# Performance work log

Measured on AMD Instinct MI355X. Metric: run time of the kernel, lower is better.

The kernel has to match this reference:

```python
import jax, jax.numpy as jnp
import numpy as np

N_NODES = 50000
N_EDGES = 400000
H = 64          # node hidden state dim (entities_dimensions['node'])
E_DIM = 8       # edge_params dim (message.extra_parameters)
MSG_HID = 128   # message-creation MLP hidden width
RD_HID = 128    # readout hidden width
T = 2           # message-passing steps


def setup_inputs() -> dict:
    key = jax.random.key(0)
    ks = jax.random.split(key, 12)
    def w(k, shape):
        return jax.random.normal(k, shape, dtype=jnp.float32) * 0.05
    return {
        "node_feats": jax.random.normal(ks[0], (N_NODES, H), dtype=jnp.float32),
        "edge_feats": jax.random.normal(ks[1], (N_EDGES, E_DIM), dtype=jnp.float32),
        "edge_src": jax.random.randint(ks[2], (N_EDGES,), 0, N_NODES),
        "edge_dst": jax.random.randint(ks[3], (N_EDGES,), 0, N_NODES),
        # message creation MLP: concat(hs_src, hs_dst, edge_params) -> relu -> H
        "W_msg1": w(ks[4], (2 * H + E_DIM, MSG_HID)),
        "b_msg1": jnp.zeros((MSG_HID,), jnp.float32),
        "W_msg2": w(ks[5], (MSG_HID, H)),
        "b_msg2": jnp.zeros((H,), jnp.float32),
        # GRU cell update (keras GRUCell convention, reset_after=False)
        "W_x": w(ks[6], (H, 3 * H)),
        "W_h": w(ks[7], (H, 3 * H)),
        "b_gru": jnp.zeros((3 * H,), jnp.float32),
        # readout MLP: H -> relu -> 1
        "W_r1": w(ks[8], (H, RD_HID)),
        "b_r1": jnp.zeros((RD_HID,), jnp.float32),
        "W_r2": w(ks[9], (RD_HID, 1)),
        "b_r2": jnp.zeros((1,), jnp.float32),
    }


def _gru_cell(h, x, W_x, W_h, b):
    # gates order: update (z), reset (r), candidate (h~) — keras convention
    gx = x @ W_x + b
    gh = h @ W_h
    xz, xr, xh = jnp.split(gx, 3, axis=-1)
    hz, hr, hh = jnp.split(gh, 3, axis=-1)
    z = jax.nn.sigmoid(xz + hz)
    r = jax.nn.sigmoid(xr + hr)
    hc = jnp.tanh(xh + r * hh)
    return z * h + (1.0 - z) * hc


def reference(node_feats, edge_feats, edge_src, edge_dst,
              W_msg1, b_msg1, W_msg2, b_msg2,
              W_x, W_h, b_gru, W_r1, b_r1, W_r2, b_r2):
    h = node_feats  # [N, H] hidden states initialized from entity features
    for _ in range(T):
        # gather source/destination node states per edge: [E, H]
        src_h = h[edge_src]
        dst_h = h[edge_dst]
        m_in = jnp.concatenate([src_h, dst_h, edge_feats], axis=-1)  # [E, 2H+E_DIM]
        m = jax.nn.relu(m_in @ W_msg1 + b_msg1) @ W_msg2 + b_msg2    # [E, H]
        # scatter-sum aggregation to destination nodes: [N, H]
        agg = jax.ops.segment_sum(m, edge_dst, num_segments=N_NODES)
        # recurrent (GRU) node-state update
        h = _gru_cell(h, agg, W_x, W_h, b_gru)
    # readout MLP on final hidden states
    out = jax.nn.relu(h @ W_r1 + b_r1) @ W_r2 + b_r2  # [N, 1]
    return out
```

## Files before the change

kernel.cpp:

```cpp
#include <hip/hip_runtime.h>
#include <hip/hip_bf16.h>

#define NN 50000
#define NE 400000
#define NPAIR 12500
#define NCH 196
#define NPAD 50176

typedef __bf16 bf16_t;
typedef __bf16 bf16x4 __attribute__((ext_vector_type(4)));
typedef __bf16 bf16x8 __attribute__((ext_vector_type(8)));
typedef float  floatx4 __attribute__((ext_vector_type(4)));

static __device__ __forceinline__ floatx4 mfma16(bf16x8 a, bf16x8 b, floatx4 c) {
    return __builtin_amdgcn_mfma_f32_16x16x32_bf16(a, b, c, 0, 0, 0);
}
static __device__ __forceinline__ float sigm_f(float x) {
    return 1.f / (1.f + __expf(-x));
}
static __device__ __forceinline__ float tanh_f(float x) {
    return 1.f - 2.f / (__expf(2.f * x) + 1.f);
}
static __device__ __forceinline__ bf16x8 cvt8(const float* sp) {
    float4 f0 = *(const float4*)sp;
    float4 f1 = *(const float4*)(sp + 4);
    bf16x8 v;
    v[0] = (bf16_t)f0.x; v[1] = (bf16_t)f0.y; v[2] = (bf16_t)f0.z; v[3] = (bf16_t)f0.w;
    v[4] = (bf16_t)f1.x; v[5] = (bf16_t)f1.y; v[6] = (bf16_t)f1.z; v[7] = (bf16_t)f1.w;
    return v;
}

__global__ __launch_bounds__(256) void prep_kernel(
    const float* __restrict__ nf,
    const float* __restrict__ Wm1, const float* __restrict__ Wm2,
    const float* __restrict__ Wx,  const float* __restrict__ Wh,
    const float* __restrict__ Wr1,
    bf16_t* __restrict__ hb,
    bf16_t* __restrict__ W1f, bf16_t* __restrict__ W2f,
    bf16_t* __restrict__ Wxt, bf16_t* __restrict__ Wht,
    bf16_t* __restrict__ Wr1f)
{
    int u = blockIdx.x * 256 + threadIdx.x;
    if (u < 800000) {
        float4 v = *(const float4*)(nf + (size_t)u * 4);
        bf16x4 o;
        o[0] = (bf16_t)v.x; o[1] = (bf16_t)v.y; o[2] = (bf16_t)v.z; o[3] = (bf16_t)v.w;
        *(bf16x4*)(hb + (size_t)u * 4) = o;
        return;
    }
    u -= 800000;
    if (u < 20480) {
        int j = u & 7, l = (u >> 3) & 63, rem = u >> 9;
        int ks = rem % 5, nt = rem / 5;
        int n = nt * 16 + (l & 15);
        int k = ks * 32 + (l >> 4) * 8 + j;
        W1f[u] = (k < 136) ? (bf16_t)Wm1[k * 128 + n] : (bf16_t)0.f;
        return;
    }
    u -= 20480;
    if (u < 8192) {
        int j = u & 7, l = (u >> 3) & 63, rem = u >> 9;
        int kg = rem & 3, nt = rem >> 2;
        int n = nt * 16 + (l & 15);
        int k = kg * 32 + (l >> 4) * 8 + j;
        W2f[u] = (bf16_t)Wm2[k * 64 + n];
        return;
    }
    u -= 8192;
    if (u < 12288) {
        int n = u >> 6, k = u & 63;
        Wxt[u] = (bf16_t)Wx[k * 192 + n];
        return;
    }
    u -= 12288;
    if (u < 12288) {
        int n = u >> 6, k = u & 63;
        Wht[u] = (bf16_t)Wh[k * 192 + n];
        return;
    }
    u -= 12288;
    if (u < 8192) {
        int j = u & 7, l = (u >> 3) & 63, rem = u >> 9;
        int kg = rem & 1, nt = rem >> 1;
        int n = nt * 16 + (l & 15);
        int k = kg * 32 + (l >> 4) * 8 + j;
        Wr1f[u] = (bf16_t)Wr1[k * 128 + n];
    }
}

__global__ __launch_bounds__(256) void hist_kernel(
    const int* __restrict__ edst, int* __restrict__ deg)
{
    int e = blockIdx.x * 256 + threadIdx.x;
    if (e < NE) atomicAdd(&deg[edst[e]], 1);
}

__global__ __launch_bounds__(256) void scanA_kernel(
    const int* __restrict__ deg, int* __restrict__ chunkSums)
{
    __shared__ int s[256];
    int i = blockIdx.x * 256 + threadIdx.x;
    s[threadIdx.x] = deg[i];
    __syncthreads();
    for (int st = 128; st >= 1; st >>= 1) {
        if (threadIdx.x < st) s[threadIdx.x] += s[threadIdx.x + st];
        __syncthreads();
    }
    if (threadIdx.x == 0) chunkSums[blockIdx.x] = s[0];
}

__global__ __launch_bounds__(256) void scanB_kernel(
    const int* __restrict__ chunkSums, int* __restrict__ chunkOff)
{
    __shared__ int s[256];
    int t = threadIdx.x;
    int v = (t < NCH) ? chunkSums[t] : 0;
    s[t] = v;
    __syncthreads();
    for (int st = 1; st < 256; st <<= 1) {
        int add = (t >= st) ? s[t - st] : 0;
        __syncthreads();
        s[t] += add;
        __syncthreads();
    }
    if (t < NCH) chunkOff[t] = s[t] - v;
}

__global__ __launch_bounds__(256) void scanC_kernel(
    const int* __restrict__ deg, const int* __restrict__ chunkOff,
    int* __restrict__ cursor)
{
    __shared__ int s[256];
    int t = threadIdx.x;
    int i = blockIdx.x * 256 + t;
    int v = deg[i];
    s[t] = v;
    __syncthreads();
    for (int st = 1; st < 256; st <<= 1) {
        int add = (t >= st) ? s[t - st] : 0;
        __syncthreads();
        s[t] += add;
        __syncthreads();
    }
    cursor[i] = chunkOff[blockIdx.x] + s[t] - v;
}

__global__ __launch_bounds__(256) void scatter_kernel(
    const int* __restrict__ esrc, const int* __restrict__ edst,
    const float* __restrict__ ef,
    int* __restrict__ cursor, int* __restrict__ srcs, int* __restrict__ dsts,
    bf16_t* __restrict__ efpb)
{
    int e = blockIdx.x * 256 + threadIdx.x;
    if (e >= NE) return;
    int d = edst[e];
    int p = atomicAdd(&cursor[d], 1);
    srcs[p] = esrc[e];
    dsts[p] = d;
    float4 a = *(const float4*)(ef + (size_t)e * 8);
    float4 b = *(const float4*)(ef + (size_t)e * 8 + 4);
    bf16x8 v;
    v[0] = (bf16_t)a.x; v[1] = (bf16_t)a.y; v[2] = (bf16_t)a.z; v[3] = (bf16_t)a.w;
    v[4] = (bf16_t)b.x; v[5] = (bf16_t)b.y; v[6] = (bf16_t)b.z; v[7] = (bf16_t)b.w;
    *(bf16x8*)(efpb + (size_t)p * 8) = v;
}

__global__ __launch_bounds__(256) void edge_kernel(
    const bf16_t* __restrict__ hb, const bf16_t* __restrict__ efpb,
    const int* __restrict__ srcs, const int* __restrict__ dsts,
    const bf16_t* __restrict__ W1f, const bf16_t* __restrict__ W2f,
    const float* __restrict__ b1f, const float* __restrict__ b2f,
    bf16_t* __restrict__ mb)
{
    __shared__ __attribute__((aligned(16))) bf16_t w1s[20480];
    __shared__ __attribute__((aligned(16))) bf16_t w2s[8192];
    __shared__ __attribute__((aligned(16))) bf16_t hq[4][32 * 36];

    const int tid = threadIdx.x;
    {
        const uint4* s1 = (const uint4*)W1f;
        uint4* d1 = (uint4*)w1s;
        #pragma unroll
        for (int i = 0; i < 10; i++) d1[tid + i * 256] = s1[tid + i * 256];
        const uint4* s2 = (const uint4*)W2f;
        uint4* d2 = (uint4*)w2s;
        #pragma unroll
        for (int i = 0; i < 4; i++) d2[tid + i * 256] = s2[tid + i * 256];
    }
    __syncthreads();

    const int lane = tid & 63;
    const int wv   = tid >> 6;
    const int l15  = lane & 15;
    const int quad = lane >> 4;

    float b1r[8], b2r[4];
    #pragma unroll
    for (int nt = 0; nt < 8; nt++) b1r[nt] = b1f[nt * 16 + l15];
    #pragma unroll
    for (int nt = 0; nt < 4; nt++) b2r[nt] = b2f[nt * 16 + l15];

    const int WTOT = gridDim.x * 4;
    int p = blockIdx.x * 4 + wv;

    bf16x8 af0[5], af1[5];
    {
        int base = p * 32;
        int r0 = base + l15, r1 = base + 16 + l15;
        int si0 = srcs[r0], di0 = dsts[r0];
        int si1 = srcs[r1], di1 = dsts[r1];
        const bf16_t* sp0 = hb + (size_t)si0 * 64 + quad * 8;
        const bf16_t* dp0 = hb + (size_t)di0 * 64 + quad * 8;
        const bf16_t* sp1 = hb + (size_t)si1 * 64 + quad * 8;
        const bf16_t* dp1 = hb + (size_t)di1 * 64 + quad * 8;
        af0[0] = *(const bf16x8*)sp0;  af0[1] = *(const bf16x8*)(sp0 + 32);
        af0[2] = *(const bf16x8*)dp0;  af0[3] = *(const bf16x8*)(dp0 + 32);
        af1[0] = *(const bf16x8*)sp1;  af1[1] = *(const bf16x8*)(sp1 + 32);
        af1[2] = *(const bf16x8*)dp1;  af1[3] = *(const bf16x8*)(dp1 + 32);
        if (quad == 0) {
            af0[4] = *(const bf16x8*)(efpb + (size_t)r0 * 8);
            af1[4] = *(const bf16x8*)(efpb + (size_t)r1 * 8);
        } else {
            #pragma unroll
            for (int q = 0; q < 8; q++) { af0[4][q] = (bf16_t)0.f; af1[4][q] = (bf16_t)0.f; }
        }
    }

    while (true) {
        int pn = p + WTOT;
        int pp = (pn < NPAIR) ? pn : p;
        int nbase = pp * 32;
        int nr0 = nbase + l15, nr1 = nbase + 16 + l15;
        int si0n = srcs[nr0], di0n = dsts[nr0];
        int si1n = srcs[nr1], di1n = dsts[nr1];

        floatx4 oa0[4], oa1[4];
        #pragma unroll
        for (int nt = 0; nt < 4; nt++) {
            oa0[nt].x=0.f; oa0[nt].y=0.f; oa0[nt].z=0.f; oa0[nt].w=0.f;
            oa1[nt].x=0.f; oa1[nt].y=0.f; oa1[nt].z=0.f; oa1[nt].w=0.f;
        }

        #pragma unroll
        for (int q = 0; q < 4; q++) {
            floatx4 ac0[2], ac1[2];
            #pragma unroll
            for (int nt = 0; nt < 2; nt++) {
                ac0[nt].x=0.f; ac0[nt].y=0.f; ac0[nt].z=0.f; ac0[nt].w=0.f;
                ac1[nt].x=0.f; ac1[nt].y=0.f; ac1[nt].z=0.f; ac1[nt].w=0.f;
            }
            #pragma unroll
            for (int nt = 0; nt < 2; nt++) {
                int gnt = q * 2 + nt;
                #pragma unroll
                for (int ks = 0; ks < 5; ks++) {
                    bf16x8 b = *(const bf16x8*)(w1s + ((gnt * 5 + ks) * 64 + lane) * 8);
                    ac0[nt] = mfma16(af0[ks], b, ac0[nt]);
                    ac1[nt] = mfma16(af1[ks], b, ac1[nt]);
                }
            }
            #pragma unroll
            for (int nt = 0; nt < 2; nt++) {
                float bb = b1r[q * 2 + nt];
                #pragma unroll
                for (int r = 0; r < 4; r++) {
                    float v0 = fmaxf(ac0[nt][r] + bb, 0.f);
                    float v1 = fmaxf(ac1[nt][r] + bb, 0.f);
                    hq[wv][(quad * 4 + r) * 36 + nt * 16 + l15]      = (bf16_t)v0;
                    hq[wv][(16 + quad * 4 + r) * 36 + nt * 16 + l15] = (bf16_t)v1;
                }
            }
            bf16x8 hf0 = *(const bf16x8*)(hq[wv] + l15 * 36 + quad * 8);
            bf16x8 hf1 = *(const bf16x8*)(hq[wv] + (16 + l15) * 36 + quad * 8);
            #pragma unroll
            for (int nt = 0; nt < 4; nt++) {
                bf16x8 w2 = *(const bf16x8*)(w2s + ((nt * 4 + q) * 64 + lane) * 8);
                oa0[nt] = mfma16(hf0, w2, oa0[nt]);
                oa1[nt] = mfma16(hf1, w2, oa1[nt]);
            }
        }

        int base = p * 32;
        {
            const bf16_t* sp0 = hb + (size_t)si0n * 64 + quad * 8;
            const bf16_t* dp0 = hb + (size_t)di0n * 64 + quad * 8;
            const bf16_t* sp1 = hb + (size_t)si1n * 64 + quad * 8;
            const bf16_t* dp1 = hb + (size_t)di1n * 64 + quad * 8;
            af0[0] = *(const bf16x8*)sp0;  af0[1] = *(const bf16x8*)(sp0 + 32);
            af0[2] = *(const bf16x8*)dp0;  af0[3] = *(const bf16x8*)(dp0 + 32);
            af1[0] = *(const bf16x8*)sp1;  af1[1] = *(const bf16x8*)(sp1 + 32);
            af1[2] = *(const bf16x8*)dp1;  af1[3] = *(const bf16x8*)(dp1 + 32);
            if (quad == 0) {
                af0[4] = *(const bf16x8*)(efpb + (size_t)nr0 * 8);
                af1[4] = *(const bf16x8*)(efpb + (size_t)nr1 * 8);
            }
        }

        #pragma unroll
        for (int nt = 0; nt < 4; nt++) {
            int col = nt * 16 + l15;
            float bb = b2r[nt];
            #pragma unroll
            for (int r = 0; r < 4; r++) {
                int row0 = base + quad * 4 + r;
                int row1 = base + 16 + quad * 4 + r;
                mb[(size_t)row0 * 64 + col] = (bf16_t)(oa0[nt][r] + bb);
                mb[(size_t)row1 * 64 + col] = (bf16_t)(oa1[nt][r] + bb);
            }
        }

        if (pn >= NPAIR) break;
        p = pn;
    }
}

__global__ __launch_bounds__(256) void agg_kernel(
    const bf16_t* __restrict__ mb, const int* __restrict__ deg,
    const int* __restrict__ cursor, bf16_t* __restrict__ aggb)
{
    const int node = blockIdx.x * 4 + (threadIdx.x >> 6);
    if (node >= NN) return;
    const int lane = threadIdx.x & 63;
    int dg  = deg[node];
    int end = cursor[node];
    int st  = end - dg;
    float s0 = 0.f, s1 = 0.f;
    int e = st;
    for (; e + 1 < end; e += 2) {
        s0 += (float)mb[(size_t)e * 64 + lane];
        s1 += (float)mb[(size_t)(e + 1) * 64 + lane];
    }
    if (e < end) s0 += (float)mb[(size_t)e * 64 + lane];
    aggb[(size_t)node * 64 + lane] = (bf16_t)(s0 + s1);
}

template<int LAST>
__global__ __launch_bounds__(256) void gru_kernel(
    const bf16_t* __restrict__ aggb, const float* __restrict__ h_in,
    float* __restrict__ h_out, bf16_t* __restrict__ hb_out,
    const bf16_t* __restrict__ Wxt, const bf16_t* __restrict__ Wht,
    const float* __restrict__ bg,
    const bf16_t* __restrict__ Wr1f, const float* __restrict__ br1,
    const float* __restrict__ Wr2, const float* __restrict__ br2,
    float* __restrict__ out)
{
    __shared__ __attribute__((aligned(16))) float  shd[64 * 68];
    __shared__ __attribute__((aligned(16))) bf16_t hb2[4][16 * 72];
    const int tid = threadIdx.x;
    const int n0  = blockIdx.x * 64;

    for (int idx = tid; idx < 64 * 16; idx += 256) {
        int i = idx >> 4, c = (idx & 15) * 4;
        int n = n0 + i; if (n >= NN) n = NN - 1;
        *(float4*)&shd[i * 68 + c] = *(const float4*)(h_in + (size_t)n * 64 + c);
    }
    __syncthreads();

    const int lane = tid & 63;
    const int wv   = tid >> 6;
    const int l15  = lane & 15;
    const int quad = lane >> 4;
    const int rowA = wv * 16 + l15;
    int nA = n0 + rowA; if (nA >= NN) nA = NN - 1;

    bf16x8 ax[2], ah[2];
    ax[0] = *(const bf16x8*)(aggb + (size_t)nA * 64 + quad * 8);
    ax[1] = *(const bf16x8*)(aggb + (size_t)nA * 64 + quad * 8 + 32);
    {
        const float* hp = shd + rowA * 68 + quad * 8;
        ah[0] = cvt8(hp);
        ah[1] = cvt8(hp + 32);
    }

    floatx4 az[4], ar[4], axh[4], ahh[4];
    #pragma unroll
    for (int nt = 0; nt < 4; nt++) {
        az[nt].x=0.f; az[nt].y=0.f; az[nt].z=0.f; az[nt].w=0.f;
        ar[nt].x=0.f; ar[nt].y=0.f; ar[nt].z=0.f; ar[nt].w=0.f;
        axh[nt].x=0.f; axh[nt].y=0.f; axh[nt].z=0.f; axh[nt].w=0.f;
        ahh[nt].x=0.f; ahh[nt].y=0.f; ahh[nt].z=0.f; ahh[nt].w=0.f;
    }
    #pragma unroll
    for (int nt = 0; nt < 4; nt++) {
        const bf16_t* bx_z = Wxt + (nt * 16 + l15) * 64 + quad * 8;
        const bf16_t* bh_z = Wht + (nt * 16 + l15) * 64 + quad * 8;
        const bf16_t* bx_r = bx_z + 64 * 64;
        const bf16_t* bh_r = bh_z + 64 * 64;
        const bf16_t* bx_h = bx_z + 128 * 64;
        const bf16_t* bh_h = bh_z + 128 * 64;
        az[nt]  = mfma16(ax[0], *(const bf16x8*)bx_z,        az[nt]);
        az[nt]  = mfma16(ax[1], *(const bf16x8*)(bx_z + 32), az[nt]);
        az[nt]  = mfma16(ah[0], *(const bf16x8*)bh_z,        az[nt]);
        az[nt]  = mfma16(ah[1], *(const bf16x8*)(bh_z + 32), az[nt]);
        ar[nt]  = mfma16(ax[0], *(const bf16x8*)bx_r,        ar[nt]);
        ar[nt]  = mfma16(ax[1], *(const bf16x8*)(bx_r + 32), ar[nt]);
        ar[nt]  = mfma16(ah[0], *(const bf16x8*)bh_r,        ar[nt]);
        ar[nt]  = mfma16(ah[1], *(const bf16x8*)(bh_r + 32), ar[nt]);
        axh[nt] = mfma16(ax[0], *(const bf16x8*)bx_h,        axh[nt]);
        axh[nt] = mfma16(ax[1], *(const bf16x8*)(bx_h + 32), axh[nt]);
        ahh[nt] = mfma16(ah[0], *(const bf16x8*)bh_h,        ahh[nt]);
        ahh[nt] = mfma16(ah[1], *(const bf16x8*)(bh_h + 32), ahh[nt]);
    }

    #pragma unroll
    for (int nt = 0; nt < 4; nt++) {
        int j = nt * 16 + l15;
        float bz = bg[j], brr = bg[64 + j], bh = bg[128 + j];
        #pragma unroll
        for (int r = 0; r < 4; r++) {
            int lrow = wv * 16 + quad * 4 + r;
            int n = n0 + lrow;
            float z  = sigm_f(az[nt][r] + bz);
            float rr = sigm_f(ar[nt][r] + brr);
            float hc = tanh_f(axh[nt][r] + bh + rr * ahh[nt][r]);
            float hold = shd[lrow * 68 + j];
            float hnew = z * hold + (1.f - z) * hc;
            if (LAST) {
                hb2[wv][(quad * 4 + r) * 72 + j] = (bf16_t)hnew;
            } else if (n < NN) {
                h_out[(size_t)n * 64 + j]  = hnew;
                hb_out[(size_t)n * 64 + j] = (bf16_t)hnew;
            }
        }
    }

    if (LAST) {
        bf16x8 a0 = *(const bf16x8*)(hb2[wv] + l15 * 72 + quad * 8);
        bf16x8 a1 = *(const bf16x8*)(hb2[wv] + l15 * 72 + quad * 8 + 32);
        floatx4 accR[8];
        #pragma unroll
        for (int nt = 0; nt < 8; nt++) { accR[nt].x=0.f; accR[nt].y=0.f; accR[nt].z=0.f; accR[nt].w=0.f; }
        #pragma unroll
        for (int nt = 0; nt < 8; nt++) {
            bf16x8 b0 = *(const bf16x8*)(Wr1f + ((nt * 2 + 0) * 64 + lane) * 8);
            bf16x8 b1 = *(const bf16x8*)(Wr1f + ((nt * 2 + 1) * 64 + lane) * 8);
            accR[nt] = mfma16(a0, b0, accR[nt]);
            accR[nt] = mfma16(a1, b1, accR[nt]);
        }
        float br1r[8], wr2r[8];
        #pragma unroll
        for (int nt = 0; nt < 8; nt++) {
            br1r[nt] = br1[nt * 16 + l15];
            wr2r[nt] = Wr2[nt * 16 + l15];
        }
        float br2v = br2[0];
        #pragma unroll
        for (int r = 0; r < 4; r++) {
            float p = 0.f;
            #pragma unroll
            for (int nt = 0; nt < 8; nt++)
                p += fmaxf(accR[nt][r] + br1r[nt], 0.f) * wr2r[nt];
            p += __shfl_xor(p, 1, 64);
            p += __shfl_xor(p, 2, 64);
            p += __shfl_xor(p, 4, 64);
            p += __shfl_xor(p, 8, 64);
            if (l15 == 0) {
                int n = n0 + wv * 16 + quad * 4 + r;
                if (n < NN) out[n] = p + br2v;
            }
        }
    }
}

extern "C" void kernel_launch(void* const* d_in, const int* in_sizes, int n_in,
                              void* d_out, int out_size, void* d_ws, size_t ws_size,
                              hipStream_t stream)
{
    const float* nf  = (const float*)d_in[0];
    const float* ef  = (const float*)d_in[1];
    const int* esrc  = (const int*)d_in[2];
    const int* edst  = (const int*)d_in[3];
    const float* Wm1 = (const float*)d_in[4];
    const float* bm1 = (const float*)d_in[5];
    const float* Wm2 = (const float*)d_in[6];
    const float* bm2 = (const float*)d_in[7];
    const float* Wx  = (const float*)d_in[8];
    const float* Wh  = (const float*)d_in[9];
    const float* bg  = (const float*)d_in[10];
    const float* Wr1 = (const float*)d_in[11];
    const float* br1 = (const float*)d_in[12];
    const float* Wr2 = (const float*)d_in[13];
    const float* br2 = (const float*)d_in[14];

    char* ws = (char*)d_ws;
    float*  hbuf   = (float*)(ws);
    bf16_t* hb     = (bf16_t*)(ws + 12800000);
    bf16_t* W1f    = (bf16_t*)(ws + 19200000);
    bf16_t* W2f    = (bf16_t*)(ws + 19240960);
    bf16_t* Wxt    = (bf16_t*)(ws + 19257344);
    bf16_t* Wht    = (bf16_t*)(ws + 19281920);
    bf16_t* Wr1f   = (bf16_t*)(ws + 19306496);
    int*    srcs   = (int*)(ws + 19322880);
    int*    dsts   = (int*)(ws + 20922880);
    bf16_t* efpb   = (bf16_t*)(ws + 22522880);
    int*    deg    = (int*)(ws + 28922880);
    int*    cursor = (int*)(ws + 29123584);
    int*    chunkS = (int*)(ws + 29324288);
    int*    chunkO = (int*)(ws + 29325312);
    bf16_t* aggb   = (bf16_t*)(ws + 29326336);
    bf16_t* mb     = (bf16_t*)(ws + 35726336);

    prep_kernel<<<3365, 256, 0, stream>>>(nf, Wm1, Wm2, Wx, Wh, Wr1,
                                          hb, W1f, W2f, Wxt, Wht, Wr1f);

    hipMemsetAsync(deg, 0, (size_t)NPAD * 4, stream);
    hist_kernel<<<(NE + 255) / 256, 256, 0, stream>>>(edst, deg);
    scanA_kernel<<<NCH, 256, 0, stream>>>(deg, chunkS);
    scanB_kernel<<<1, 256, 0, stream>>>(chunkS, chunkO);
    scanC_kernel<<<NCH, 256, 0, stream>>>(deg, chunkO, cursor);
    scatter_kernel<<<(NE + 255) / 256, 256, 0, stream>>>(esrc, edst, ef, cursor,
                                                         srcs, dsts, efpb);

    edge_kernel<<<1024, 256, 0, stream>>>(hb, efpb, srcs, dsts,
                                          W1f, W2f, bm1, bm2, mb);
    agg_kernel<<<(NN + 3) / 4, 256, 0, stream>>>(mb, deg, cursor, aggb);
    gru_kernel<0><<<(NN + 63) / 64, 256, 0, stream>>>(
        aggb, nf, hbuf, hb, Wxt, Wht, bg, Wr1f, br1, Wr2, br2, (float*)d_out);
    edge_kernel<<<1024, 256, 0, stream>>>(hb, efpb, srcs, dsts,
                                          W1f, W2f, bm1, bm2, mb);
    agg_kernel<<<(NN + 3) / 4, 256, 0, stream>>>(mb, deg, cursor, aggb);
    gru_kernel<1><<<(NN + 63) / 64, 256, 0, stream>>>(
        aggb, hbuf, nullptr, nullptr, Wxt, Wht, bg, Wr1f, br1, Wr2, br2,
        (float*)d_out);
}
```

Before: 324.6 us.

## Process 64 edges per wave, permute message columns, vectorize aggregation, fuse histogram

The edge kernel now processes four 16-row tiles (64 edges) per wave, so each shared-memory weight fragment feeds four MFMAs instead of two. The W2 columns are permuted so each lane writes a packed bf16x4 of messages and packed bf16x2 hidden values. The aggregation kernel reads bf16x4 per lane across four edges in parallel and reduces with shuffles. The degree histogram is folded into the prep kernel and the edge grid is halved. This raises register pressure per wave and leaves fewer waves for load balancing.

```diff
diff --git a/kernel.cpp b/kernel.cpp
--- a/kernel.cpp
+++ b/kernel.cpp
@@ -3,11 +3,12 @@
 
 #define NN 50000
 #define NE 400000
-#define NPAIR 12500
+#define NUNIT 6250
 #define NCH 196
 #define NPAD 50176
 
 typedef __bf16 bf16_t;
+typedef __bf16 bf16x2 __attribute__((ext_vector_type(2)));
 typedef __bf16 bf16x4 __attribute__((ext_vector_type(4)));
 typedef __bf16 bf16x8 __attribute__((ext_vector_type(8)));
 typedef float  floatx4 __attribute__((ext_vector_type(4)));
@@ -35,6 +36,7 @@
     const float* __restrict__ Wm1, const float* __restrict__ Wm2,
     const float* __restrict__ Wx,  const float* __restrict__ Wh,
     const float* __restrict__ Wr1,
+    const int* __restrict__ edst, int* __restrict__ deg,
     bf16_t* __restrict__ hb,
     bf16_t* __restrict__ W1f, bf16_t* __restrict__ W2f,
     bf16_t* __restrict__ Wxt, bf16_t* __restrict__ Wht,
@@ -62,7 +64,8 @@
         int j = u & 7, l = (u >> 3) & 63, rem = u >> 9;
         int kg = rem & 3, nt = rem >> 2;
         int n = nt * 16 + (l & 15);
-        int k = kg * 32 + (l >> 4) * 8 + j;
+        int local = (l >> 4) * 8 + j;
+        int k = kg * 32 + (local >> 1) + (local & 1) * 16;
         W2f[u] = (bf16_t)Wm2[k * 64 + n];
         return;
     }
@@ -85,14 +88,10 @@
         int n = nt * 16 + (l & 15);
         int k = kg * 32 + (l >> 4) * 8 + j;
         Wr1f[u] = (bf16_t)Wr1[k * 128 + n];
-    }
-}
-
-__global__ __launch_bounds__(256) void hist_kernel(
-    const int* __restrict__ edst, int* __restrict__ deg)
-{
-    int e = blockIdx.x * 256 + threadIdx.x;
-    if (e < NE) atomicAdd(&deg[edst[e]], 1);
+        return;
+    }
+    u -= 8192;
+    if (u < NE) atomicAdd(&deg[edst[u]], 1);
 }
 
 __global__ __launch_bounds__(256) void scanA_kernel(
@@ -165,7 +164,7 @@
     *(bf16x8*)(efpb + (size_t)p * 8) = v;
 }
 
-__global__ __launch_bounds__(256) void edge_kernel(
+__global__ __launch_bounds__(256, 2) void edge_kernel(
     const bf16_t* __restrict__ hb, const bf16_t* __restrict__ efpb,
     const int* __restrict__ srcs, const int* __restrict__ dsts,
     const bf16_t* __restrict__ W1f, const bf16_t* __restrict__ W2f,
@@ -174,7 +173,7 @@
 {
     __shared__ __attribute__((aligned(16))) bf16_t w1s[20480];
     __shared__ __attribute__((aligned(16))) bf16_t w2s[8192];
-    __shared__ __attribute__((aligned(16))) bf16_t hq[4][32 * 36];
+    __shared__ __attribute__((aligned(16))) bf16_t hq[4][64 * 36];
 
     const int tid = threadIdx.x;
     {
@@ -203,113 +202,117 @@
     const int WTOT = gridDim.x * 4;
     int p = blockIdx.x * 4 + wv;
 
-    bf16x8 af0[5], af1[5];
+    bf16x8 af[4][5];
     {
-        int base = p * 32;
-        int r0 = base + l15, r1 = base + 16 + l15;
-        int si0 = srcs[r0], di0 = dsts[r0];
-        int si1 = srcs[r1], di1 = dsts[r1];
-        const bf16_t* sp0 = hb + (size_t)si0 * 64 + quad * 8;
-        const bf16_t* dp0 = hb + (size_t)di0 * 64 + quad * 8;
-        const bf16_t* sp1 = hb + (size_t)si1 * 64 + quad * 8;
-        const bf16_t* dp1 = hb + (size_t)di1 * 64 + quad * 8;
-        af0[0] = *(const bf16x8*)sp0;  af0[1] = *(const bf16x8*)(sp0 + 32);
-        af0[2] = *(const bf16x8*)dp0;  af0[3] = *(const bf16x8*)(dp0 + 32);
-        af1[0] = *(const bf16x8*)sp1;  af1[1] = *(const bf16x8*)(sp1 + 32);
-        af1[2] = *(const bf16x8*)dp1;  af1[3] = *(const bf16x8*)(dp1 + 32);
-        if (quad == 0) {
-            af0[4] = *(const bf16x8*)(efpb + (size_t)r0 * 8);
-            af1[4] = *(const bf16x8*)(efpb + (size_t)r1 * 8);
-        } else {
-            #pragma unroll
-            for (int q = 0; q < 8; q++) { af0[4][q] = (bf16_t)0.f; af1[4][q] = (bf16_t)0.f; }
+        int base = p * 64;
+        #pragma unroll
+        for (int s = 0; s < 4; s++) {
+            int r = base + s * 16 + l15;
+            int si = srcs[r], di = dsts[r];
+            const bf16_t* sp = hb + (size_t)si * 64 + quad * 8;
+            const bf16_t* dp = hb + (size_t)di * 64 + quad * 8;
+            af[s][0] = *(const bf16x8*)sp;  af[s][1] = *(const bf16x8*)(sp + 32);
+            af[s][2] = *(const bf16x8*)dp;  af[s][3] = *(const bf16x8*)(dp + 32);
+            if (quad == 0) {
+                af[s][4] = *(const bf16x8*)(efpb + (size_t)r * 8);
+            } else {
+                #pragma unroll
+                for (int q = 0; q < 8; q++) af[s][4][q] = (bf16_t)0.f;
+            }
         }
     }
 
     while (true) {
         int pn = p + WTOT;
-        int pp = (pn < NPAIR) ? pn : p;
-        int nbase = pp * 32;
-        int nr0 = nbase + l15, nr1 = nbase + 16 + l15;
-        int si0n = srcs[nr0], di0n = dsts[nr0];
-        int si1n = srcs[nr1], di1n = dsts[nr1];
-
-        floatx4 oa0[4], oa1[4];
-        #pragma unroll
-        for (int nt = 0; nt < 4; nt++) {
-            oa0[nt].x=0.f; oa0[nt].y=0.f; oa0[nt].z=0.f; oa0[nt].w=0.f;
-            oa1[nt].x=0.f; oa1[nt].y=0.f; oa1[nt].z=0.f; oa1[nt].w=0.f;
-        }
+        int pp = (pn < NUNIT) ? pn : p;
+        int nbase = pp * 64;
+        int sin[4], din[4];
+        #pragma unroll
+        for (int s = 0; s < 4; s++) {
+            sin[s] = srcs[nbase + s * 16 + l15];
+            din[s] = dsts[nbase + s * 16 + l15];
+        }
+
+        floatx4 oa[4][4];
+        #pragma unroll
+        for (int s = 0; s < 4; s++)
+            #pragma unroll
+            for (int nt = 0; nt < 4; nt++) {
+                oa[s][nt].x=0.f; oa[s][nt].y=0.f; oa[s][nt].z=0.f; oa[s][nt].w=0.f;
+            }
 
         #pragma unroll
         for (int q = 0; q < 4; q++) {
-            floatx4 ac0[2], ac1[2];
-            #pragma unroll
-            for (int nt = 0; nt < 2; nt++) {
-                ac0[nt].x=0.f; ac0[nt].y=0.f; ac0[nt].z=0.f; ac0[nt].w=0.f;
-                ac1[nt].x=0.f; ac1[nt].y=0.f; ac1[nt].z=0.f; ac1[nt].w=0.f;
-            }
+            floatx4 ac[4][2];
+            #pragma unroll
+            for (int s = 0; s < 4; s++)
+                #pragma unroll
+                for (int nt = 0; nt < 2; nt++) {
+                    ac[s][nt].x=0.f; ac[s][nt].y=0.f; ac[s][nt].z=0.f; ac[s][nt].w=0.f;
+                }
             #pragma unroll
             for (int nt = 0; nt < 2; nt++) {
                 int gnt = q * 2 + nt;
                 #pragma unroll
                 for (int ks = 0; ks < 5; ks++) {
                     bf16x8 b = *(const bf16x8*)(w1s + ((gnt * 5 + ks) * 64 + lane) * 8);
-                    ac0[nt] = mfma16(af0[ks], b, ac0[nt]);
-                    ac1[nt] = mfma16(af1[ks], b, ac1[nt]);
+                    #pragma unroll
+                    for (int s = 0; s < 4; s++)
+                        ac[s][nt] = mfma16(af[s][ks], b, ac[s][nt]);
                 }
             }
-            #pragma unroll
-            for (int nt = 0; nt < 2; nt++) {
-                float bb = b1r[q * 2 + nt];
+            {
+                float bb0 = b1r[q * 2 + 0], bb1 = b1r[q * 2 + 1];
                 #pragma unroll
-                for (int r = 0; r < 4; r++) {
-                    float v0 = fmaxf(ac0[nt][r] + bb, 0.f);
-                    float v1 = fmaxf(ac1[nt][r] + bb, 0.f);
-                    hq[wv][(quad * 4 + r) * 36 + nt * 16 + l15]      = (bf16_t)v0;
-                    hq[wv][(16 + quad * 4 + r) * 36 + nt * 16 + l15] = (bf16_t)v1;
+                for (int s = 0; s < 4; s++) {
+                    #pragma unroll
+                    for (int r = 0; r < 4; r++) {
+                        float v0 = fmaxf(ac[s][0][r] + bb0, 0.f);
+                        float v1 = fmaxf(ac[s][1][r] + bb1, 0.f);
+                        bf16x2 t; t[0] = (bf16_t)v0; t[1] = (bf16_t)v1;
+                        *(bf16x2*)(hq[wv] + (s * 16 + quad * 4 + r) * 36 + l15 * 2) = t;
+                    }
                 }
             }
-            bf16x8 hf0 = *(const bf16x8*)(hq[wv] + l15 * 36 + quad * 8);
-            bf16x8 hf1 = *(const bf16x8*)(hq[wv] + (16 + l15) * 36 + quad * 8);
+            bf16x8 hf[4];
+            #pragma unroll
+            for (int s = 0; s < 4; s++)
+                hf[s] = *(const bf16x8*)(hq[wv] + (s * 16 + l15) * 36 + quad * 8);
             #pragma unroll
             for (int nt = 0; nt < 4; nt++) {
                 bf16x8 w2 = *(const bf16x8*)(w2s + ((nt * 4 + q) * 64 + lane) * 8);
-                oa0[nt] = mfma16(hf0, w2, oa0[nt]);
-                oa1[nt] = mfma16(hf1, w2, oa1[nt]);
-            }
-        }
-
-        int base = p * 32;
-        {
-            const bf16_t* sp0 = hb + (size_t)si0n * 64 + quad * 8;
-            const bf16_t* dp0 = hb + (size_t)di0n * 64 + quad * 8;
-            const bf16_t* sp1 = hb + (size_t)si1n * 64 + quad * 8;
-            const bf16_t* dp1 = hb + (size_t)di1n * 64 + quad * 8;
-            af0[0] = *(const bf16x8*)sp0;  af0[1] = *(const bf16x8*)(sp0 + 32);
-            af0[2] = *(const bf16x8*)dp0;  af0[3] = *(const bf16x8*)(dp0 + 32);
-            af1[0] = *(const bf16x8*)sp1;  af1[1] = *(const bf16x8*)(sp1 + 32);
-            af1[2] = *(const bf16x8*)dp1;  af1[3] = *(const bf16x8*)(dp1 + 32);
-            if (quad == 0) {
-                af0[4] = *(const bf16x8*)(efpb + (size_t)nr0 * 8);
-                af1[4] = *(const bf16x8*)(efpb + (size_t)nr1 * 8);
-            }
-        }
-
-        #pragma unroll
-        for (int nt = 0; nt < 4; nt++) {
-            int col = nt * 16 + l15;
-            float bb = b2r[nt];
+                #pragma unroll
+                for (int s = 0; s < 4; s++)
+                    oa[s][nt] = mfma16(hf[s], w2, oa[s][nt]);
+            }
+        }
+
+        int base = p * 64;
+        #pragma unroll
+        for (int s = 0; s < 4; s++) {
+            const bf16_t* sp = hb + (size_t)sin[s] * 64 + quad * 8;
+            const bf16_t* dp = hb + (size_t)din[s] * 64 + quad * 8;
+            af[s][0] = *(const bf16x8*)sp;  af[s][1] = *(const bf16x8*)(sp + 32);
+            af[s][2] = *(const bf16x8*)dp;  af[s][3] = *(const bf16x8*)(dp + 32);
+            if (quad == 0)
+                af[s][4] = *(const bf16x8*)(efpb + (size_t)(nbase + s * 16 + l15) * 8);
+        }
+
+        #pragma unroll
+        for (int s = 0; s < 4; s++) {
             #pragma unroll
             for (int r = 0; r < 4; r++) {
-                int row0 = base + quad * 4 + r;
-                int row1 = base + 16 + quad * 4 + r;
-                mb[(size_t)row0 * 64 + col] = (bf16_t)(oa0[nt][r] + bb);
-                mb[(size_t)row1 * 64 + col] = (bf16_t)(oa1[nt][r] + bb);
-            }
-        }
-
-        if (pn >= NPAIR) break;
+                int row = base + s * 16 + quad * 4 + r;
+                bf16x4 t;
+                t[0] = (bf16_t)(oa[s][0][r] + b2r[0]);
+                t[1] = (bf16_t)(oa[s][1][r] + b2r[1]);
+                t[2] = (bf16_t)(oa[s][2][r] + b2r[2]);
+                t[3] = (bf16_t)(oa[s][3][r] + b2r[3]);
+                *(bf16x4*)(mb + (size_t)row * 64 + l15 * 4) = t;
+            }
+        }
+
+        if (pn >= NUNIT) break;
         p = pn;
     }
 }
@@ -321,17 +324,26 @@
     const int node = blockIdx.x * 4 + (threadIdx.x >> 6);
     if (node >= NN) return;
     const int lane = threadIdx.x & 63;
+    const int l15  = lane & 15;
+    const int quad = lane >> 4;
     int dg  = deg[node];
     int end = cursor[node];
     int st  = end - dg;
-    float s0 = 0.f, s1 = 0.f;
-    int e = st;
-    for (; e + 1 < end; e += 2) {
-        s0 += (float)mb[(size_t)e * 64 + lane];
-        s1 += (float)mb[(size_t)(e + 1) * 64 + lane];
-    }
-    if (e < end) s0 += (float)mb[(size_t)e * 64 + lane];
-    aggb[(size_t)node * 64 + lane] = (bf16_t)(s0 + s1);
+    float a0 = 0.f, a1 = 0.f, a2 = 0.f, a3 = 0.f;
+    for (int e = st + quad; e < end; e += 4) {
+        bf16x4 v = *(const bf16x4*)(mb + (size_t)e * 64 + l15 * 4);
+        a0 += (float)v[0]; a1 += (float)v[1]; a2 += (float)v[2]; a3 += (float)v[3];
+    }
+    a0 += __shfl_xor(a0, 16, 64); a0 += __shfl_xor(a0, 32, 64);
+    a1 += __shfl_xor(a1, 16, 64); a1 += __shfl_xor(a1, 32, 64);
+    a2 += __shfl_xor(a2, 16, 64); a2 += __shfl_xor(a2, 32, 64);
+    a3 += __shfl_xor(a3, 16, 64); a3 += __shfl_xor(a3, 32, 64);
+    if (quad == 0) {
+        aggb[(size_t)node * 64 +      l15] = (bf16_t)a0;
+        aggb[(size_t)node * 64 + 16 + l15] = (bf16_t)a1;
+        aggb[(size_t)node * 64 + 32 + l15] = (bf16_t)a2;
+        aggb[(size_t)node * 64 + 48 + l15] = (bf16_t)a3;
+    }
 }
 
 template<int LAST>
@@ -500,24 +512,23 @@
     bf16_t* aggb   = (bf16_t*)(ws + 29326336);
     bf16_t* mb     = (bf16_t*)(ws + 35726336);
 
-    prep_kernel<<<3365, 256, 0, stream>>>(nf, Wm1, Wm2, Wx, Wh, Wr1,
+    hipMemsetAsync(deg, 0, (size_t)NPAD * 4, stream);
+    prep_kernel<<<4928, 256, 0, stream>>>(nf, Wm1, Wm2, Wx, Wh, Wr1, edst, deg,
                                           hb, W1f, W2f, Wxt, Wht, Wr1f);
 
-    hipMemsetAsync(deg, 0, (size_t)NPAD * 4, stream);
-    hist_kernel<<<(NE + 255) / 256, 256, 0, stream>>>(edst, deg);
     scanA_kernel<<<NCH, 256, 0, stream>>>(deg, chunkS);
     scanB_kernel<<<1, 256, 0, stream>>>(chunkS, chunkO);
     scanC_kernel<<<NCH, 256, 0, stream>>>(deg, chunkO, cursor);
     scatter_kernel<<<(NE + 255) / 256, 256, 0, stream>>>(esrc, edst, ef, cursor,
                                                          srcs, dsts, efpb);
 
-    edge_kernel<<<1024, 256, 0, stream>>>(hb, efpb, srcs, dsts,
-                                          W1f, W2f, bm1, bm2, mb);
+    edge_kernel<<<512, 256, 0, stream>>>(hb, efpb, srcs, dsts,
+                                         W1f, W2f, bm1, bm2, mb);
     agg_kernel<<<(NN + 3) / 4, 256, 0, stream>>>(mb, deg, cursor, aggb);
     gru_kernel<0><<<(NN + 63) / 64, 256, 0, stream>>>(
         aggb, nf, hbuf, hb, Wxt, Wht, bg, Wr1f, br1, Wr2, br2, (float*)d_out);
-    edge_kernel<<<1024, 256, 0, stream>>>(hb, efpb, srcs, dsts,
-                                          W1f, W2f, bm1, bm2, mb);
+    edge_kernel<<<512, 256, 0, stream>>>(hb, efpb, srcs, dsts,
+                                         W1f, W2f, bm1, bm2, mb);
     agg_kernel<<<(NN + 3) / 4, 256, 0, stream>>>(mb, deg, cursor, aggb);
     gru_kernel<1><<<(NN + 63) / 64, 256, 0, stream>>>(
         aggb, hbuf, nullptr, nullptr, Wxt, Wht, bg, Wr1f, br1, Wr2, br2,
```

New measurement: 372.0 us. 14.6% more time.

## Drop W2 from LDS, pack hidden stores, fuse histogram into prep kernel

Applied to the files above, without the earlier changes.

The edge kernel no longer stages W_msg2 in shared memory; it reads the fragments straight from global memory, which should be L2-resident. This shrinks LDS use so that three blocks fit per CU (launch bounds 3, grid 768). The W2 fragment layout is permuted so each lane can write its two relu outputs to the hq tile as one bf16x2 store instead of two scalar stores. The degree histogram is folded into the prep kernel to remove a launch. The risk is higher latency from the global W2 loads inside the hot loop.

```diff
diff --git a/kernel.cpp b/kernel.cpp
--- a/kernel.cpp
+++ b/kernel.cpp
@@ -8,6 +8,7 @@
 #define NPAD 50176
 
 typedef __bf16 bf16_t;
+typedef __bf16 bf16x2 __attribute__((ext_vector_type(2)));
 typedef __bf16 bf16x4 __attribute__((ext_vector_type(4)));
 typedef __bf16 bf16x8 __attribute__((ext_vector_type(8)));
 typedef float  floatx4 __attribute__((ext_vector_type(4)));
@@ -35,6 +36,7 @@
     const float* __restrict__ Wm1, const float* __restrict__ Wm2,
     const float* __restrict__ Wx,  const float* __restrict__ Wh,
     const float* __restrict__ Wr1,
+    const int* __restrict__ edst, int* __restrict__ deg,
     bf16_t* __restrict__ hb,
     bf16_t* __restrict__ W1f, bf16_t* __restrict__ W2f,
     bf16_t* __restrict__ Wxt, bf16_t* __restrict__ Wht,
@@ -62,7 +64,8 @@
         int j = u & 7, l = (u >> 3) & 63, rem = u >> 9;
         int kg = rem & 3, nt = rem >> 2;
         int n = nt * 16 + (l & 15);
-        int k = kg * 32 + (l >> 4) * 8 + j;
+        int local = (l >> 4) * 8 + j;
+        int k = kg * 32 + (local >> 1) + (local & 1) * 16;
         W2f[u] = (bf16_t)Wm2[k * 64 + n];
         return;
     }
@@ -85,14 +88,10 @@
         int n = nt * 16 + (l & 15);
         int k = kg * 32 + (l >> 4) * 8 + j;
         Wr1f[u] = (bf16_t)Wr1[k * 128 + n];
-    }
-}
-
-__global__ __launch_bounds__(256) void hist_kernel(
-    const int* __restrict__ edst, int* __restrict__ deg)
-{
-    int e = blockIdx.x * 256 + threadIdx.x;
-    if (e < NE) atomicAdd(&deg[edst[e]], 1);
+        return;
+    }
+    u -= 8192;
+    if (u < NE) atomicAdd(&deg[edst[u]], 1);
 }
 
 __global__ __launch_bounds__(256) void scanA_kernel(
@@ -165,7 +164,7 @@
     *(bf16x8*)(efpb + (size_t)p * 8) = v;
 }
 
-__global__ __launch_bounds__(256) void edge_kernel(
+__global__ __launch_bounds__(256, 3) void edge_kernel(
     const bf16_t* __restrict__ hb, const bf16_t* __restrict__ efpb,
     const int* __restrict__ srcs, const int* __restrict__ dsts,
     const bf16_t* __restrict__ W1f, const bf16_t* __restrict__ W2f,
@@ -173,7 +172,6 @@
     bf16_t* __restrict__ mb)
 {
     __shared__ __attribute__((aligned(16))) bf16_t w1s[20480];
-    __shared__ __attribute__((aligned(16))) bf16_t w2s[8192];
     __shared__ __attribute__((aligned(16))) bf16_t hq[4][32 * 36];
 
     const int tid = threadIdx.x;
@@ -182,10 +180,6 @@
         uint4* d1 = (uint4*)w1s;
         #pragma unroll
         for (int i = 0; i < 10; i++) d1[tid + i * 256] = s1[tid + i * 256];
-        const uint4* s2 = (const uint4*)W2f;
-        uint4* d2 = (uint4*)w2s;
-        #pragma unroll
-        for (int i = 0; i < 4; i++) d2[tid + i * 256] = s2[tid + i * 256];
     }
     __syncthreads();
 
@@ -259,22 +253,25 @@
                     ac1[nt] = mfma16(af1[ks], b, ac1[nt]);
                 }
             }
-            #pragma unroll
-            for (int nt = 0; nt < 2; nt++) {
-                float bb = b1r[q * 2 + nt];
+            {
+                float bb0 = b1r[q * 2 + 0], bb1 = b1r[q * 2 + 1];
                 #pragma unroll
                 for (int r = 0; r < 4; r++) {
-                    float v0 = fmaxf(ac0[nt][r] + bb, 0.f);
-                    float v1 = fmaxf(ac1[nt][r] + bb, 0.f);
-                    hq[wv][(quad * 4 + r) * 36 + nt * 16 + l15]      = (bf16_t)v0;
-                    hq[wv][(16 + quad * 4 + r) * 36 + nt * 16 + l15] = (bf16_t)v1;
+                    float v00 = fmaxf(ac0[0][r] + bb0, 0.f);
+                    float v01 = fmaxf(ac0[1][r] + bb1, 0.f);
+                    bf16x2 t0; t0[0] = (bf16_t)v00; t0[1] = (bf16_t)v01;
+                    *(bf16x2*)(hq[wv] + (quad * 4 + r) * 36 + l15 * 2) = t0;
+                    float v10 = fmaxf(ac1[0][r] + bb0, 0.f);
+                    float v11 = fmaxf(ac1[1][r] + bb1, 0.f);
+                    bf16x2 t1; t1[0] = (bf16_t)v10; t1[1] = (bf16_t)v11;
+                    *(bf16x2*)(hq[wv] + (16 + quad * 4 + r) * 36 + l15 * 2) = t1;
                 }
             }
             bf16x8 hf0 = *(const bf16x8*)(hq[wv] + l15 * 36 + quad * 8);
             bf16x8 hf1 = *(const bf16x8*)(hq[wv] + (16 + l15) * 36 + quad * 8);
             #pragma unroll
             for (int nt = 0; nt < 4; nt++) {
-                bf16x8 w2 = *(const bf16x8*)(w2s + ((nt * 4 + q) * 64 + lane) * 8);
+                bf16x8 w2 = *(const bf16x8*)(W2f + ((size_t)((nt * 4 + q) * 64 + lane)) * 8);
                 oa0[nt] = mfma16(hf0, w2, oa0[nt]);
                 oa1[nt] = mfma16(hf1, w2, oa1[nt]);
             }
@@ -500,24 +497,23 @@
     bf16_t* aggb   = (bf16_t*)(ws + 29326336);
     bf16_t* mb     = (bf16_t*)(ws + 35726336);
 
-    prep_kernel<<<3365, 256, 0, stream>>>(nf, Wm1, Wm2, Wx, Wh, Wr1,
+    hipMemsetAsync(deg, 0, (size_t)NPAD * 4, stream);
+    prep_kernel<<<4928, 256, 0, stream>>>(nf, Wm1, Wm2, Wx, Wh, Wr1, edst, deg,
                                           hb, W1f, W2f, Wxt, Wht, Wr1f);
 
-    hipMemsetAsync(deg, 0, (size_t)NPAD * 4, stream);
-    hist_kernel<<<(NE + 255) / 256, 256, 0, stream>>>(edst, deg);
     scanA_kernel<<<NCH, 256, 0, stream>>>(deg, chunkS);
     scanB_kernel<<<1, 256, 0, stream>>>(chunkS, chunkO);
     scanC_kernel<<<NCH, 256, 0, stream>>>(deg, chunkO, cursor);
     scatter_kernel<<<(NE + 255) / 256, 256, 0, stream>>>(esrc, edst, ef, cursor,
                                                          srcs, dsts, efpb);
 
-    edge_kernel<<<1024, 256, 0, stream>>>(hb, efpb, srcs, dsts,
-                                          W1f, W2f, bm1, bm2, mb);
+    edge_kernel<<<768, 256, 0, stream>>>(hb, efpb, srcs, dsts,
+                                         W1f, W2f, bm1, bm2, mb);
     agg_kernel<<<(NN + 3) / 4, 256, 0, stream>>>(mb, deg, cursor, aggb);
     gru_kernel<0><<<(NN + 63) / 64, 256, 0, stream>>>(
         aggb, nf, hbuf, hb, Wxt, Wht, bg, Wr1f, br1, Wr2, br2, (float*)d_out);
-    edge_kernel<<<1024, 256, 0, stream>>>(hb, efpb, srcs, dsts,
-                                          W1f, W2f, bm1, bm2, mb);
+    edge_kernel<<<768, 256, 0, stream>>>(hb, efpb, srcs, dsts,
+                                         W1f, W2f, bm1, bm2, mb);
     agg_kernel<<<(NN + 3) / 4, 256, 0, stream>>>(mb, deg, cursor, aggb);
     gru_kernel<1><<<(NN + 63) / 64, 256, 0, stream>>>(
         aggb, hbuf, nullptr, nullptr, Wxt, Wht, bg, Wr1f, br1, Wr2, br2,
```

After: 515.0 us. +58.7%, slower.
